# Kernel optimization log

Hardware: AMD Instinct MI355X
Metric: run time of the kernel (lower is better)

The kernel has to match this reference:

```python
import jax, jax.numpy as jnp
import numpy as np

B, S, D = 256, 512, 512

def setup_inputs() -> dict:
    key = jax.random.key(0)
    k1, k2, k3 = jax.random.split(key, 3)
    x = jax.random.normal(k1, (B, S), dtype=jnp.float32)
    # per-position Dense(1 -> D): stacked kernels [S, D] and biases [S, D]
    # glorot_uniform for fan_in=1, fan_out=D: limit = sqrt(6/(1+D))
    limit = np.sqrt(6.0 / (1 + D)).astype(np.float32)
    W = jax.random.uniform(k2, (S, D), dtype=jnp.float32, minval=-limit, maxval=limit)
    b = jnp.zeros((S, D), dtype=jnp.float32) + 0.0 * jax.random.normal(k3, (S, D), dtype=jnp.float32)
    return {"x": x, "W": W, "b": b}

def reference(x, W, b):
    # Fused equivalent of seq_length separate Dense(1->D)+Dropout calls.
    # out[b,i,:] = relu(x[b,i] * W[i,:] + b[i,:]); dropout is identity in eval mode.
    out = jax.nn.relu(x[:, :, None] * W[None, :, :] + b[None, :, :])  # [B, S, D]
    return out
```

## Files before the change

### kernel.cpp

```cpp
#include <hip/hip_runtime.h>


constexpr int B = 256;
constexpr int S = 512;
constexpr int D = 512;
constexpr int D4 = D / 4;
constexpr int TOTAL4 = B * S * D4;

__global__ void __launch_bounds__(256) od2d_kernel(
    const float* __restrict__ x,
    const float4* __restrict__ W4,
    const float4* __restrict__ b4,
    float4* __restrict__ o4)
{
    const unsigned stride = gridDim.x * blockDim.x;
    for (unsigned i = blockIdx.x * blockDim.x + threadIdx.x; i < TOTAL4; i += stride) {
        const unsigned d4 = i & (D4 - 1);
        const unsigned bs = i >> 7;
        const unsigned s  = bs & (S - 1);
        const float xv = x[bs];
        const unsigned wi = (s << 7) + d4;
        const float4 w  = W4[wi];
        const float4 bb = b4[wi];
        float4 r;
        r.x = fmaxf(fmaf(xv, w.x, bb.x), 0.0f);
        r.y = fmaxf(fmaf(xv, w.y, bb.y), 0.0f);
        r.z = fmaxf(fmaf(xv, w.z, bb.z), 0.0f);
        r.w = fmaxf(fmaf(xv, w.w, bb.w), 0.0f);
        o4[i] = r;
    }
}

extern "C" void kernel_launch(void* const* d_in, const int* in_sizes, int n_in,
                              void* d_out, int out_size, void* d_ws, size_t ws_size,
                              hipStream_t stream) {
    const float*  x  = (const float*)d_in[0];
    const float4* W4 = (const float4*)d_in[1];
    const float4* b4 = (const float4*)d_in[2];
    float4* o4 = (float4*)d_out;

    const int block = 256;
    const int grid  = 2048;
    od2d_kernel<<<grid, block, 0, stream>>>(x, W4, b4, o4);
}
```

Measured before the change: 49.94 us.

## Hoist W/b loads out of grid-stride loop, unroll, and use nontemporal stores

Because the grid stride (2048*256 float4s = 4096 rows) is a multiple of S*D4, each thread always touches the same W/b element, so W and b are loaded once per thread instead of on every iteration. The loop becomes a fully unrolled 32-iteration fixed loop that only reloads x and writes output. Output stores are marked nontemporal to avoid polluting cache with the 256MB write stream. This hardcodes the launch geometry and shape, so the indexing is only correct for this exact grid size.

```diff
diff --git a/kernel.cpp b/kernel.cpp
--- a/kernel.cpp
+++ b/kernel.cpp
@@ -1,45 +1,50 @@
 #include <hip/hip_runtime.h>
 
 
-constexpr int B = 256;
-constexpr int S = 512;
-constexpr int D = 512;
-constexpr int D4 = D / 4;
-constexpr int TOTAL4 = B * S * D4;
+typedef float __attribute__((ext_vector_type(4))) floatx4;
+
+constexpr int D4      = 128;
+constexpr int THREADS = 2048 * 256;
+constexpr int ITERS   = 32;
 
 __global__ void __launch_bounds__(256) od2d_kernel(
-    const float* __restrict__ x,
-    const float4* __restrict__ W4,
-    const float4* __restrict__ b4,
-    float4* __restrict__ o4)
+    const float*   __restrict__ x,
+    const floatx4* __restrict__ W4,
+    const floatx4* __restrict__ b4,
+    floatx4*       __restrict__ o4)
 {
-    const unsigned stride = gridDim.x * blockDim.x;
-    for (unsigned i = blockIdx.x * blockDim.x + threadIdx.x; i < TOTAL4; i += stride) {
-        const unsigned d4 = i & (D4 - 1);
-        const unsigned bs = i >> 7;
-        const unsigned s  = bs & (S - 1);
+    const unsigned t   = blockIdx.x * 256 + threadIdx.x;
+    const unsigned d4  = t & (D4 - 1);
+    const unsigned bs0 = t >> 7;
+    const unsigned s   = bs0 & 511;
+    const unsigned wi  = (s << 7) + d4;
+
+    const floatx4 w  = W4[wi];
+    const floatx4 bb = b4[wi];
+
+    unsigned i  = t;
+    unsigned bs = bs0;
+    #pragma unroll
+    for (int k = 0; k < ITERS; ++k) {
         const float xv = x[bs];
-        const unsigned wi = (s << 7) + d4;
-        const float4 w  = W4[wi];
-        const float4 bb = b4[wi];
-        float4 r;
+        floatx4 r;
         r.x = fmaxf(fmaf(xv, w.x, bb.x), 0.0f);
         r.y = fmaxf(fmaf(xv, w.y, bb.y), 0.0f);
         r.z = fmaxf(fmaf(xv, w.z, bb.z), 0.0f);
         r.w = fmaxf(fmaf(xv, w.w, bb.w), 0.0f);
-        o4[i] = r;
+        __builtin_nontemporal_store(r, &o4[i]);
+        i  += THREADS;
+        bs += 4096;
     }
 }
 
 extern "C" void kernel_launch(void* const* d_in, const int* in_sizes, int n_in,
                               void* d_out, int out_size, void* d_ws, size_t ws_size,
                               hipStream_t stream) {
-    const float*  x  = (const float*)d_in[0];
-    const float4* W4 = (const float4*)d_in[1];
-    const float4* b4 = (const float4*)d_in[2];
-    float4* o4 = (float4*)d_out;
+    const float*   x  = (const float*)d_in[0];
+    const floatx4* W4 = (const floatx4*)d_in[1];
+    const floatx4* b4 = (const floatx4*)d_in[2];
+    floatx4* o4 = (floatx4*)d_out;
 
-    const int block = 256;
-    const int grid  = 2048;
-    od2d_kernel<<<grid, block, 0, stream>>>(x, W4, b4, o4);
+    od2d_kernel<<<2048, 256, 0, stream>>>(x, W4, b4, o4);
 }
```

Measured after the change: 65.18 us. 1.31x slower.
